# Kernel optimization log

Measured on AMD Instinct MI355X. Metric: run time of the kernel, lower is better.

## Reference

```python
import jax, jax.numpy as jnp
import numpy as np

TEMP = 8.0  # softmax temperature from softmax_(X, N=8.0)
EPS = 1e-12  # F.normalize eps


def qmul(q, r):
    # Hamilton product, quaternions stored as (w, x, y, z); broadcasts over leading dims.
    w1, x1, y1, z1 = q[..., 0], q[..., 1], q[..., 2], q[..., 3]
    w2, x2, y2, z2 = r[..., 0], r[..., 1], r[..., 2], r[..., 3]
    return jnp.stack([
        w1 * w2 - x1 * x2 - y1 * y2 - z1 * z2,
        w1 * x2 + x1 * w2 + y1 * z2 - z1 * y2,
        w1 * y2 - x1 * z2 + y1 * w2 + z1 * x2,
        w1 * z2 + x1 * y2 - y1 * x2 + z1 * w2,
    ], axis=-1)


def setup_inputs() -> dict:
    key = jax.random.key(0)
    kl, kq, krq, kw, ks, kd = jax.random.split(key, 6)
    N, K, E = 100000, 8, 3200000
    node_levels = jax.random.uniform(kl, (N, K), dtype=jnp.float32)
    node_q = jax.random.normal(kq, (N, K, 4), dtype=jnp.float32)
    node_q = node_q / jnp.linalg.norm(node_q, axis=-1, keepdims=True)
    edge_rel_q = jax.random.normal(krq, (E, 4), dtype=jnp.float32)
    edge_rel_q = edge_rel_q / jnp.linalg.norm(edge_rel_q, axis=-1, keepdims=True)
    edge_w = jax.random.uniform(kw, (E,), dtype=jnp.float32)
    edge_src = jax.random.randint(ks, (E,), 0, N, dtype=jnp.int32)
    edge_dst = jax.random.randint(kd, (E,), 0, N, dtype=jnp.int32)
    return {"node_levels": node_levels, "node_q": node_q, "edge_rel_q": edge_rel_q,
            "edge_w": edge_w, "edge_src": edge_src, "edge_dst": edge_dst}


def reference(node_levels, node_q, edge_rel_q, edge_w, edge_src, edge_dst):
    N, K = node_levels.shape
    # --- gather (DGL message_func): per-edge source features ---
    q_src = node_q[edge_src]          # [E,K,4]
    l_src = node_levels[edge_src]     # [E,K]
    # accumulated quaternion: rel_q (broadcast over K) * neighbor q
    accu_q = qmul(edge_rel_q[:, None, :], q_src)  # [E,K,4]

    # --- distance-weighted softmax over {self} U in-neighbors, per (node, k) ---
    score_e = TEMP * edge_w[:, None] * l_src      # [E,K]  edge term: w * l
    score_s = TEMP * node_levels                  # [N,K]  self term: w=1
    seg_max = jax.ops.segment_max(score_e, edge_dst, num_segments=N)  # -inf if no in-edges
    m = jnp.maximum(seg_max, score_s)             # [N,K] stable max incl. self
    exp_e = jnp.exp(score_e - m[edge_dst])
    exp_s = jnp.exp(score_s - m)
    denom = jax.ops.segment_sum(exp_e, edge_dst, num_segments=N) + exp_s  # [N,K]
    w_e = exp_e / denom[edge_dst]                 # [E,K]
    w_s = exp_s / denom                           # [N,K]

    # --- weighted aggregation (scatter) ---
    out_q = jax.ops.segment_sum(w_e[..., None] * accu_q, edge_dst, num_segments=N) \
            + w_s[..., None] * node_q             # [N,K,4]
    out_levels = jax.ops.segment_sum(w_e * l_src, edge_dst, num_segments=N) \
            + w_s * node_levels                   # [N,K]

    # F.normalize(p=2, dim=-1) with eps clamp
    norm = jnp.maximum(jnp.linalg.norm(out_q, axis=-1, keepdims=True), EPS)
    q = out_q / norm
    return q, out_levels
```

## Files before the change

### kernel.cpp

```cpp
#include <hip/hip_runtime.h>
#include <hip/hip_fp16.h>

#define TEMP 8.0f
#define MSHIFT 8.0f
#define KDIM 8

__device__ __forceinline__ unsigned pack_h2(float a, float b) {
    __half2 h = __floats2half2_rn(a, b);
    return __builtin_bit_cast(unsigned, h);
}
__device__ __forceinline__ float2 unpack_h2(unsigned v) {
    __half2 h = __builtin_bit_cast(__half2, v);
    return __half22float2(h);
}

__global__ void nodepack(const float* __restrict__ levels,
                         const float4* __restrict__ node_q,
                         float4* __restrict__ packed, int NK) {
    int i = blockIdx.x * blockDim.x + threadIdx.x;
    if (i >= NK) return;
    float4 q = node_q[i];
    uint4 u;
    u.x = pack_h2(q.x, q.y);
    u.y = pack_h2(q.z, q.w);
    u.z = __builtin_bit_cast(unsigned, levels[i]);
    u.w = 0;
    packed[i] = __builtin_bit_cast(float4, u);
}

__global__ void bucket_scatter(const int* __restrict__ edst,
                               const int* __restrict__ esrc,
                               const float* __restrict__ ew,
                               const float4* __restrict__ rel_q,
                               int* __restrict__ deg,
                               float4* __restrict__ payload,
                               int CAP, int E) {
    int e = blockIdx.x * blockDim.x + threadIdx.x;
    if (e >= E) return;
    int dst = edst[e];
    int pos = atomicAdd(&deg[dst], 1);
    if (pos >= CAP) return;
    float4 r = rel_q[e];
    uint4 u;
    u.x = pack_h2(r.x, r.y);
    u.y = pack_h2(r.z, r.w);
    u.z = __builtin_bit_cast(unsigned, TEMP * ew[e]);
    u.w = (unsigned)(esrc[e] * KDIM);
    payload[(size_t)dst * CAP + pos] = __builtin_bit_cast(float4, u);
}

__global__ void agg_wave(const float* __restrict__ levels,
                         const float4* __restrict__ node_q,
                         const float4* __restrict__ packed,
                         const int* __restrict__ deg,
                         const float4* __restrict__ payload,
                         int CAP,
                         float4* __restrict__ out_q,
                         float* __restrict__ out_lvl, int N) {
    int t = blockIdx.x * blockDim.x + threadIdx.x;
    int n = t >> 6;
    if (n >= N) return;
    int lane = t & 63;
    int k = lane & 7;
    int seg = lane >> 3;

    float den = 0.f, lv = 0.f, aw = 0.f, ax = 0.f, ay = 0.f, az = 0.f;

    int cnt = deg[n];
    if (cnt > CAP) cnt = CAP;
    const float4* bp = payload + (size_t)n * CAP;
#pragma unroll 2
    for (int j = seg; j < cnt; j += 8) {
        float4 pe = bp[j];
        uint4 pu = __builtin_bit_cast(uint4, pe);
        float2 r01 = unpack_h2(pu.x);
        float2 r23 = unpack_h2(pu.y);
        float tw = pe.z;
        int src8 = __builtin_bit_cast(int, pu.w);
        float4 nd = packed[src8 + k];
        uint4 nu = __builtin_bit_cast(uint4, nd);
        float2 q01 = unpack_h2(nu.x);
        float2 q23 = unpack_h2(nu.y);
        float ls = nd.z;
        float ex = __expf(tw * ls - MSHIFT);
        den += ex;
        lv += ex * ls;
        float rw = r01.x, rx = r01.y, ry = r23.x, rz = r23.y;
        float qw = q01.x, qx = q01.y, qy = q23.x, qz = q23.y;
        aw += ex * (rw * qw - rx * qx - ry * qy - rz * qz);
        ax += ex * (rw * qx + rx * qw + ry * qz - rz * qy);
        ay += ex * (rw * qy - rx * qz + ry * qw + rz * qx);
        az += ex * (rw * qz + rx * qy - ry * qx + rz * qw);
    }

#pragma unroll
    for (int m = 8; m <= 32; m <<= 1) {
        den += __shfl_xor(den, m, 64);
        lv  += __shfl_xor(lv,  m, 64);
        aw  += __shfl_xor(aw,  m, 64);
        ax  += __shfl_xor(ax,  m, 64);
        ay  += __shfl_xor(ay,  m, 64);
        az  += __shfl_xor(az,  m, 64);
    }

    if (seg == 0) {
        int i = n * KDIM + k;
        float l = levels[i];
        float es = __expf(TEMP * l - MSHIFT);
        den += es;
        lv += es * l;
        float4 q0 = node_q[i];
        aw += es * q0.x; ax += es * q0.y; ay += es * q0.z; az += es * q0.w;

        float inv = 1.0f / den;
        lv *= inv; aw *= inv; ax *= inv; ay *= inv; az *= inv;
        float nn = sqrtf(aw * aw + ax * ax + ay * ay + az * az);
        nn = fmaxf(nn, 1e-12f);
        float rn = 1.0f / nn;
        float4 o;
        o.x = aw * rn; o.y = ax * rn; o.z = ay * rn; o.w = az * rn;
        out_q[i] = o;
        out_lvl[i] = lv;
    }
}


__global__ void rank_kernel(const int* __restrict__ edst, int* __restrict__ deg,
                            int* __restrict__ rank, int E) {
    int e = blockIdx.x * blockDim.x + threadIdx.x;
    if (e < E) rank[e] = atomicAdd(&deg[edst[e]], 1);
}

__global__ void scan1(const int* __restrict__ deg, int* __restrict__ offs,
                      int* __restrict__ bsum, int N) {
    __shared__ int s[256];
    int i = blockIdx.x * 256 + threadIdx.x;
    int v = (i < N) ? deg[i] : 0;
    s[threadIdx.x] = v;
    __syncthreads();
    for (int off = 1; off < 256; off <<= 1) {
        int t = (threadIdx.x >= off) ? s[threadIdx.x - off] : 0;
        __syncthreads();
        s[threadIdx.x] += t;
        __syncthreads();
    }
    if (i < N) offs[i] = s[threadIdx.x] - v;
    if (threadIdx.x == 255) bsum[blockIdx.x] = s[255];
}

__global__ void scan2(int* __restrict__ bsum, int nb) {
    __shared__ int s[1024];
    __shared__ int carry_s;
    if (threadIdx.x == 0) carry_s = 0;
    __syncthreads();
    for (int base = 0; base < nb; base += 1024) {
        int idx = base + threadIdx.x;
        int v = (idx < nb) ? bsum[idx] : 0;
        s[threadIdx.x] = v;
        __syncthreads();
        for (int off = 1; off < 1024; off <<= 1) {
            int t = (threadIdx.x >= off) ? s[threadIdx.x - off] : 0;
            __syncthreads();
            s[threadIdx.x] += t;
            __syncthreads();
        }
        if (idx < nb) bsum[idx] = s[threadIdx.x] - v + carry_s;
        __syncthreads();
        if (threadIdx.x == 0) carry_s += s[1023];
        __syncthreads();
    }
}

__global__ void scan3(int* __restrict__ offs, const int* __restrict__ bsum,
                      int N, int E) {
    int i = blockIdx.x * 256 + threadIdx.x;
    if (i < N) offs[i] += bsum[blockIdx.x];
    if (i == 0) offs[N] = E;
}

__global__ void permute_kernel(const int* __restrict__ edst,
                               const int* __restrict__ rank,
                               const int* __restrict__ offs,
                               const float4* __restrict__ rel_q,
                               const float* __restrict__ ew,
                               const int* __restrict__ esrc,
                               float4* __restrict__ payload, int E) {
    int e = blockIdx.x * blockDim.x + threadIdx.x;
    if (e >= E) return;
    int pos = offs[edst[e]] + rank[e];
    payload[2 * pos] = rel_q[e];
    float4 m;
    m.x = TEMP * ew[e];
    m.y = __int_as_float(esrc[e] * KDIM);
    m.z = 0.0f; m.w = 0.0f;
    payload[2 * pos + 1] = m;
}

__global__ void agg_payload(const float* __restrict__ levels,
                            const float4* __restrict__ node_q,
                            const int* __restrict__ offs,
                            const float4* __restrict__ payload,
                            float4* __restrict__ out_q,
                            float* __restrict__ out_lvl, int N) {
    int t = blockIdx.x * blockDim.x + threadIdx.x;
    int n = t >> 3;
    int k = t & 7;
    if (n >= N) return;
    int i = n * KDIM + k;
    float l = levels[i];
    float es = __expf(TEMP * l - MSHIFT);
    float den = es, lv = es * l;
    float4 q0 = node_q[i];
    float aw = es * q0.x, ax = es * q0.y, ay = es * q0.z, az = es * q0.w;
    int beg = offs[n], end = offs[n + 1];
#pragma unroll 2
    for (int j = beg; j < end; j++) {
        float4 r = payload[2 * j];
        float4 m = payload[2 * j + 1];
        float tw = m.x;
        int src8 = __float_as_int(m.y);
        float ls = levels[src8 + k];
        float ex = __expf(tw * ls - MSHIFT);
        float4 q = node_q[src8 + k];
        den += ex;
        lv += ex * ls;
        aw += ex * (r.x * q.x - r.y * q.y - r.z * q.z - r.w * q.w);
        ax += ex * (r.x * q.y + r.y * q.x + r.z * q.w - r.w * q.z);
        ay += ex * (r.x * q.z - r.y * q.w + r.z * q.x + r.w * q.y);
        az += ex * (r.x * q.w + r.y * q.z - r.z * q.y + r.w * q.x);
    }
    float inv = 1.0f / den;
    lv *= inv; aw *= inv; ax *= inv; ay *= inv; az *= inv;
    float nn = sqrtf(aw * aw + ax * ax + ay * ay + az * az);
    nn = fmaxf(nn, 1e-12f);
    float rn = 1.0f / nn;
    float4 o;
    o.x = aw * rn; o.y = ax * rn; o.z = ay * rn; o.w = az * rn;
    out_q[i] = o;
    out_lvl[i] = lv;
}

extern "C" void kernel_launch(void* const* d_in, const int* in_sizes, int n_in,
                              void* d_out, int out_size, void* d_ws, size_t ws_size,
                              hipStream_t stream) {
    const float*  levels = (const float*)d_in[0];
    const float4* node_q = (const float4*)d_in[1];
    const float4* rel_q  = (const float4*)d_in[2];
    const float*  ew     = (const float*)d_in[3];
    const int*    esrc   = (const int*)d_in[4];
    const int*    edst   = (const int*)d_in[5];

    const int NK = in_sizes[0];
    const int E  = in_sizes[3];
    const int N  = NK / KDIM;
    const int B  = 256;
    const int gE = (E + B - 1) / B;
    const int gN = (NK + B - 1) / B;

    float* out_q   = (float*)d_out;
    float* out_lvl = (float*)d_out + (size_t)NK * 4;

    size_t deg_bytes  = ((size_t)N * 4 + 255) & ~(size_t)255;
    size_t pack_bytes = ((size_t)NK * 16 + 255) & ~(size_t)255;
    long long cap_avail = 0;
    if (ws_size > deg_bytes + pack_bytes)
        cap_avail = (long long)((ws_size - deg_bytes - pack_bytes) / ((size_t)N * 16));
    int CAP = (cap_avail > 96) ? 96 : (int)cap_avail;

    if (CAP >= 80) {
        int* deg = (int*)d_ws;
        float4* packed  = (float4*)((char*)d_ws + deg_bytes);
        float4* payload = (float4*)((char*)d_ws + deg_bytes + pack_bytes);
        (void)hipMemsetAsync(deg, 0, (size_t)N * sizeof(int), stream);
        nodepack<<<gN, B, 0, stream>>>(levels, node_q, packed, NK);
        bucket_scatter<<<gE, B, 0, stream>>>(edst, esrc, ew, rel_q, deg, payload,
                                             CAP, E);
        int gW = (int)(((size_t)N * 64 + B - 1) / B);
        agg_wave<<<gW, B, 0, stream>>>(levels, node_q, packed, deg, payload, CAP,
                                       (float4*)out_q, out_lvl, N);
        return;
    }

    const int nb = (N + 255) / 256;
    int* deg  = (int*)d_ws;
    int* offs = deg + N;
    int* bsum = offs + N + 1;
    size_t prefix = (size_t)(2 * N + 1 + nb);
    int* rank = bsum + nb;
    size_t pay_off = (prefix + E + 3) & ~(size_t)3;
    float4* payload = (float4*)((int*)d_ws + pay_off);

    (void)hipMemsetAsync(deg, 0, (size_t)N * sizeof(int), stream);
    rank_kernel<<<gE, B, 0, stream>>>(edst, deg, rank, E);
    scan1<<<nb, 256, 0, stream>>>(deg, offs, bsum, N);
    scan2<<<1, 1024, 0, stream>>>(bsum, nb);
    scan3<<<nb, 256, 0, stream>>>(offs, bsum, N, E);
    permute_kernel<<<gE, B, 0, stream>>>(edst, rank, offs, rel_q, ew, esrc,
                                         payload, E);
    agg_payload<<<gN, B, 0, stream>>>(levels, node_q, offs, payload,
                                      (float4*)out_q, out_lvl, N);
}
```

Before: 342.9 us.

## Fuse prep kernels, pad degree counters, and use nontemporal payload loads

Merges the node-packing and edge-bucketing kernels into one launch split by block index, which removes a kernel launch and lets both phases overlap. Each per-node degree counter now sits on its own 64-byte slot, so atomics on nearby destinations no longer contend on the same cache line. The aggregation kernel reads degrees and the edge payload with nontemporal loads so this streaming data does not push the reused node table out of cache. The padding makes the memset and the workspace footprint for the counters sixteen times larger, and it reduces the per-node payload capacity left in the workspace.

```diff
diff --git a/kernel.cpp b/kernel.cpp
--- a/kernel.cpp
+++ b/kernel.cpp
@@ -4,6 +4,9 @@
 #define TEMP 8.0f
 #define MSHIFT 8.0f
 #define KDIM 8
+#define DEGS 16
+
+typedef int nt_i4 __attribute__((ext_vector_type(4)));
 
 __device__ __forceinline__ unsigned pack_h2(float a, float b) {
     __half2 h = __floats2half2_rn(a, b);
@@ -14,39 +17,40 @@
     return __half22float2(h);
 }
 
-__global__ void nodepack(const float* __restrict__ levels,
-                         const float4* __restrict__ node_q,
-                         float4* __restrict__ packed, int NK) {
-    int i = blockIdx.x * blockDim.x + threadIdx.x;
-    if (i >= NK) return;
-    float4 q = node_q[i];
-    uint4 u;
-    u.x = pack_h2(q.x, q.y);
-    u.y = pack_h2(q.z, q.w);
-    u.z = __builtin_bit_cast(unsigned, levels[i]);
-    u.w = 0;
-    packed[i] = __builtin_bit_cast(float4, u);
-}
-
-__global__ void bucket_scatter(const int* __restrict__ edst,
-                               const int* __restrict__ esrc,
-                               const float* __restrict__ ew,
-                               const float4* __restrict__ rel_q,
-                               int* __restrict__ deg,
-                               float4* __restrict__ payload,
-                               int CAP, int E) {
-    int e = blockIdx.x * blockDim.x + threadIdx.x;
-    if (e >= E) return;
-    int dst = edst[e];
-    int pos = atomicAdd(&deg[dst], 1);
-    if (pos >= CAP) return;
-    float4 r = rel_q[e];
-    uint4 u;
-    u.x = pack_h2(r.x, r.y);
-    u.y = pack_h2(r.z, r.w);
-    u.z = __builtin_bit_cast(unsigned, TEMP * ew[e]);
-    u.w = (unsigned)(esrc[e] * KDIM);
-    payload[(size_t)dst * CAP + pos] = __builtin_bit_cast(float4, u);
+__global__ void prep_fused(const float* __restrict__ levels,
+                           const float4* __restrict__ node_q,
+                           float4* __restrict__ packed, int NK, int gN,
+                           const int* __restrict__ edst,
+                           const int* __restrict__ esrc,
+                           const float* __restrict__ ew,
+                           const float4* __restrict__ rel_q,
+                           int* __restrict__ deg,
+                           float4* __restrict__ payload,
+                           int CAP, int E) {
+    if ((int)blockIdx.x < gN) {
+        int i = blockIdx.x * blockDim.x + threadIdx.x;
+        if (i >= NK) return;
+        float4 q = node_q[i];
+        uint4 u;
+        u.x = pack_h2(q.x, q.y);
+        u.y = pack_h2(q.z, q.w);
+        u.z = __builtin_bit_cast(unsigned, levels[i]);
+        u.w = 0;
+        packed[i] = __builtin_bit_cast(float4, u);
+    } else {
+        int e = (blockIdx.x - gN) * blockDim.x + threadIdx.x;
+        if (e >= E) return;
+        int dst = edst[e];
+        int pos = atomicAdd(&deg[dst * DEGS], 1);
+        if (pos >= CAP) return;
+        float4 r = rel_q[e];
+        uint4 u;
+        u.x = pack_h2(r.x, r.y);
+        u.y = pack_h2(r.z, r.w);
+        u.z = __builtin_bit_cast(unsigned, TEMP * ew[e]);
+        u.w = (unsigned)(esrc[e] * KDIM);
+        payload[(size_t)dst * CAP + pos] = __builtin_bit_cast(float4, u);
+    }
 }
 
 __global__ void agg_wave(const float* __restrict__ levels,
@@ -66,16 +70,16 @@
 
     float den = 0.f, lv = 0.f, aw = 0.f, ax = 0.f, ay = 0.f, az = 0.f;
 
-    int cnt = deg[n];
+    int cnt = __builtin_nontemporal_load(deg + (size_t)n * DEGS);
     if (cnt > CAP) cnt = CAP;
     const float4* bp = payload + (size_t)n * CAP;
 #pragma unroll 2
     for (int j = seg; j < cnt; j += 8) {
-        float4 pe = bp[j];
-        uint4 pu = __builtin_bit_cast(uint4, pe);
+        nt_i4 pv = __builtin_nontemporal_load((const nt_i4*)(bp + j));
+        uint4 pu = __builtin_bit_cast(uint4, pv);
         float2 r01 = unpack_h2(pu.x);
         float2 r23 = unpack_h2(pu.y);
-        float tw = pe.z;
+        float tw = __builtin_bit_cast(float, pu.z);
         int src8 = __builtin_bit_cast(int, pu.w);
         float4 nd = packed[src8 + k];
         uint4 nu = __builtin_bit_cast(uint4, nd);
@@ -260,7 +264,7 @@
     float* out_q   = (float*)d_out;
     float* out_lvl = (float*)d_out + (size_t)NK * 4;
 
-    size_t deg_bytes  = ((size_t)N * 4 + 255) & ~(size_t)255;
+    size_t deg_bytes  = ((size_t)N * DEGS * 4 + 255) & ~(size_t)255;
     size_t pack_bytes = ((size_t)NK * 16 + 255) & ~(size_t)255;
     long long cap_avail = 0;
     if (ws_size > deg_bytes + pack_bytes)
@@ -271,10 +275,10 @@
         int* deg = (int*)d_ws;
         float4* packed  = (float4*)((char*)d_ws + deg_bytes);
         float4* payload = (float4*)((char*)d_ws + deg_bytes + pack_bytes);
-        (void)hipMemsetAsync(deg, 0, (size_t)N * sizeof(int), stream);
-        nodepack<<<gN, B, 0, stream>>>(levels, node_q, packed, NK);
-        bucket_scatter<<<gE, B, 0, stream>>>(edst, esrc, ew, rel_q, deg, payload,
-                                             CAP, E);
+        (void)hipMemsetAsync(deg, 0, (size_t)N * DEGS * sizeof(int), stream);
+        prep_fused<<<gN + gE, B, 0, stream>>>(levels, node_q, packed, NK, gN,
+                                              edst, esrc, ew, rel_q, deg, payload,
+                                              CAP, E);
         int gW = (int)(((size_t)N * 64 + B - 1) / B);
         agg_wave<<<gW, B, 0, stream>>>(levels, node_q, packed, deg, payload, CAP,
                                        (float4*)out_q, out_lvl, N);
```

After: 348.8 us. About the same (+1.7%).
